# Kernel optimization log

Measured on AMD Instinct MI355X. Metric: run time of the kernel, lower is better.

The kernel has to match this reference:

```python
import jax, jax.numpy as jnp
import numpy as np

S = 64   # feature-map height/width = sqrt(qvk_dim)
M = 2    # memory_block_size


def _block_divide(t):
    # (b, c, S*S) -> (b, c, (S/M)**2, M*M), matching
    # Rearrange('b c (h m1) (w m2) -> b c (h w) (m1 m2)')
    b, c, _ = t.shape
    h = S // M
    t = t.reshape(b, c, h, M, h, M)
    t = jnp.transpose(t, (0, 1, 2, 4, 3, 5))
    return t.reshape(b, c, h * h, M * M)


def setup_inputs() -> dict:
    key = jax.random.key(0)
    k1, k2, k3, k4 = jax.random.split(key, 4)
    B, C, F = 64, 64, S * S
    x = jax.random.normal(k1, (B, C, F), dtype=jnp.float32)
    scale = 1.0 / np.sqrt(F)
    Wq = jax.random.normal(k2, (F, F), dtype=jnp.float32) * scale
    Wk = jax.random.normal(k3, (F, F), dtype=jnp.float32) * scale
    Wv = jax.random.normal(k4, (F, F), dtype=jnp.float32) * scale
    return {"x": x, "Wq": Wq, "Wk": Wk, "Wv": Wv}


def reference(x, Wq, Wk, Wv):
    # Linear(in, out, bias=False): y = x @ W.T, W: (out, in)
    q = _block_divide(jnp.einsum('bcf,qf->bcq', x, Wq))  # (b,c,n,g)
    k = _block_divide(jnp.einsum('bcf,qf->bcq', x, Wk))  # (b,c,n,p)
    v = _block_divide(jnp.einsum('bcf,qf->bcq', x, Wv))  # (b,c,n,p)
    # score[b,c,n,g,p] = q[b,c,n,g] * k[b,c,n,p]; softmax over p (dim=4)
    score = q[..., :, None] * k[..., None, :]             # (b,c,n,g,p)
    att = jax.nn.softmax(score, axis=-1)
    # matmul(att (g,p), v (p,1)) -> (g,1), then flatten blocks
    out = jnp.einsum('bcngp,bcnp->bcng', att, v)          # (b,c,n,g)
    b, c, n, g = out.shape
    return out.reshape(b, c, n * g)
```

## Files before the change

### kernel.cpp

```cpp
#include <hip/hip_runtime.h>

#define F        4096
#define NE       ((size_t)F * F)

typedef __attribute__((ext_vector_type(8))) short bf16x8;
typedef __attribute__((ext_vector_type(4))) float f32x4;

typedef const void __attribute__((address_space(1)))* gas1p;
typedef void __attribute__((address_space(3)))*       as3p;

__device__ __forceinline__ void gload16(const void* g, void* l) {
    __builtin_amdgcn_global_load_lds((gas1p)g, (as3p)l, 16, 0, 0);
}

__device__ __forceinline__ unsigned short f2bf(float f) {
    union { float f; unsigned int u; } c; c.f = f;
    unsigned int u = c.u;
    u += 0x7fffu + ((u >> 16) & 1u);
    return (unsigned short)(u >> 16);
}
__device__ __forceinline__ float bf2f(unsigned short u) {
    union { unsigned int u; float f; } c; c.u = ((unsigned int)u) << 16;
    return c.f;
}

__global__ void cvt_f32_bf16(const float* __restrict__ in,
                             unsigned short* __restrict__ out, int n4) {
    int idx    = blockIdx.x * blockDim.x + threadIdx.x;
    int stride = gridDim.x * blockDim.x;
    const float4* in4 = (const float4*)in;
    ushort4* out4 = (ushort4*)out;
    for (int i = idx; i < n4; i += stride) {
        float4 v = in4[i];
        ushort4 o;
        o.x = f2bf(v.x); o.y = f2bf(v.y); o.z = f2bf(v.z); o.w = f2bf(v.w);
        out4[i] = o;
    }
}

__device__ __forceinline__ int qo_map(int o) {
    int nblk = o >> 2, g = o & 3;
    return (nblk >> 5) * 128 + (g >> 1) * 64 + (nblk & 31) * 2 + (g & 1);
}

#define MFMA16(a, b, c) __builtin_amdgcn_mfma_f32_16x16x32_bf16(a, b, c, 0, 0, 0)

#define GBM 256
#define GBN 256
#define GBK 32
#define NKT (F / GBK)
#define ELPS (GBM * GBK)

__launch_bounds__(512, 1)
__global__ void gemm_qkv(const unsigned short* __restrict__ Xb,
                         const unsigned short* __restrict__ Qw,
                         const unsigned short* __restrict__ Kw,
                         const unsigned short* __restrict__ Vw,
                         unsigned short* __restrict__ qkv) {
    __shared__ __align__(16) unsigned short Als[4][GBM][GBK];
    __shared__ __align__(16) unsigned short Bls[4][GBN][GBK];

    const int tid  = threadIdx.x;
    const int lane = tid & 63;
    const int wid  = tid >> 6;
    const int wm   = wid >> 2;
    const int wn   = wid & 3;

    const int bid = blockIdx.x;
    const int swz = (bid & 7) * 96 + (bid >> 3);
    const int mt  = swz & 15;
    const int nt  = swz >> 4;
    const int bm  = mt * GBM;
    const int bnG = nt * GBN;
    const int mat = bnG >> 12;
    const int bn  = bnG & 4095;
    const unsigned short* __restrict__ Wsel = (mat == 0) ? Qw : (mat == 1) ? Kw : Vw;

    const int sr_row = tid >> 2;
    const int sr_chn = (tid & 3) ^ ((tid >> 3) & 3);
    const unsigned short* aSrc0 = Xb + (size_t)(bm + sr_row) * F + sr_chn * 8;
    const unsigned short* aSrc1 = aSrc0 + (size_t)128 * F;
    const unsigned short* bSrc0 = Wsel + (size_t)qo_map(bn + sr_row) * F + sr_chn * 8;
    const unsigned short* bSrc1 = Wsel + (size_t)qo_map(bn + 128 + sr_row) * F + sr_chn * 8;

#define STAGE_A(s, tt) do {                                                   \
        gload16(aSrc0 + (size_t)(tt) * GBK, (void*)&Als[s][wid * 16][0]);     \
        gload16(aSrc1 + (size_t)(tt) * GBK, (void*)&Als[s][128 + wid * 16][0]); \
    } while (0)
#define STAGE_B(s, tt) do {                                                   \
        gload16(bSrc0 + (size_t)(tt) * GBK, (void*)&Bls[s][wid * 16][0]);     \
        gload16(bSrc1 + (size_t)(tt) * GBK, (void*)&Bls[s][128 + wid * 16][0]); \
    } while (0)

    const int fr  = lane & 15;
    const int fq  = lane >> 4;
    const int fq2 = fq ^ ((fr >> 1) & 3);
    const unsigned short* aRd = &Als[0][wm * 128 + fr][fq2 * 8];
    const unsigned short* bRd = &Bls[0][wn * 64 + fr][fq2 * 8];

    f32x4 acc[8][4];
#pragma unroll
    for (int m = 0; m < 8; ++m)
#pragma unroll
        for (int n = 0; n < 4; ++n)
            acc[m][n] = (f32x4){0.f, 0.f, 0.f, 0.f};

    STAGE_A(0, 0); STAGE_B(0, 0);
    STAGE_A(1, 1); STAGE_B(1, 1);
    STAGE_A(2, 2); STAGE_B(2, 2);
    asm volatile("s_waitcnt vmcnt(8)" ::: "memory");
    __builtin_amdgcn_s_barrier();
    __builtin_amdgcn_sched_barrier(0);

#pragma unroll 4
    for (int t = 0; t < NKT; ++t) {
        const int s  = t & 3;
        const int ns = (t + 3) & 3;
        const int tt = (t + 3) & (NKT - 1);
        const unsigned short* aS = aRd + s * ELPS;
        const unsigned short* bS = bRd + s * ELPS;

        bf16x8 bf[4];
#pragma unroll
        for (int n = 0; n < 4; ++n) bf[n] = *(const bf16x8*)(bS + n * 512);
        bf16x8 af[4];
#pragma unroll
        for (int m = 0; m < 4; ++m) af[m] = *(const bf16x8*)(aS + m * 512);
        STAGE_A(ns, tt);
        __builtin_amdgcn_sched_barrier(0);
        __builtin_amdgcn_s_barrier();
        __builtin_amdgcn_s_setprio(1);
#pragma unroll
        for (int m = 0; m < 4; ++m)
#pragma unroll
            for (int n = 0; n < 4; ++n)
                acc[m][n] = MFMA16(af[m], bf[n], acc[m][n]);
        __builtin_amdgcn_s_setprio(0);
        __builtin_amdgcn_sched_barrier(0);
        __builtin_amdgcn_s_barrier();

#pragma unroll
        for (int m = 0; m < 4; ++m) af[m] = *(const bf16x8*)(aS + (4 + m) * 512);
        STAGE_B(ns, tt);
        __builtin_amdgcn_sched_barrier(0);
        __builtin_amdgcn_s_barrier();
        __builtin_amdgcn_s_setprio(1);
#pragma unroll
        for (int m = 0; m < 4; ++m)
#pragma unroll
            for (int n = 0; n < 4; ++n)
                acc[4 + m][n] = MFMA16(af[m], bf[n], acc[4 + m][n]);
        __builtin_amdgcn_s_setprio(0);
        asm volatile("s_waitcnt vmcnt(8)" ::: "memory");
        __builtin_amdgcn_sched_barrier(0);
        __builtin_amdgcn_s_barrier();
    }

    unsigned short* outB = qkv + (size_t)mat * NE;
#pragma unroll
    for (int m = 0; m < 8; ++m) {
#pragma unroll
        for (int n = 0; n < 4; ++n) {
#pragma unroll
            for (int r = 0; r < 4; ++r) {
                int row = bm + wm * 128 + m * 16 + fq * 4 + r;
                int col = bn + wn * 64 + n * 16 + fr;
                outB[(size_t)row * F + col] = f2bf(acc[m][n][r]);
            }
        }
    }
#undef STAGE_A
#undef STAGE_B
}

__global__ void attn_ep(const unsigned short* __restrict__ qkv,
                        float* __restrict__ out) {
    const size_t NB = NE / 4;
    const ushort4* q4 = (const ushort4*)qkv;
    const ushort4* k4 = q4 + NB;
    const ushort4* v4 = k4 + NB;
    float4* o4 = (float4*)out;
    size_t i      = (size_t)blockIdx.x * blockDim.x + threadIdx.x;
    size_t stride = (size_t)gridDim.x * blockDim.x;
    for (; i < NB; i += stride) {
        ushort4 qu = q4[i], ku = k4[i], vu = v4[i];
        float q0 = bf2f(qu.x), q1 = bf2f(qu.y), q2 = bf2f(qu.z), q3 = bf2f(qu.w);
        float k0 = bf2f(ku.x), k1 = bf2f(ku.y), k2 = bf2f(ku.z), k3 = bf2f(ku.w);
        float v0 = bf2f(vu.x), v1 = bf2f(vu.y), v2 = bf2f(vu.z), v3 = bf2f(vu.w);
        float4 res;
#pragma unroll
        for (int g = 0; g < 4; ++g) {
            float qg = (g == 0) ? q0 : (g == 1) ? q1 : (g == 2) ? q2 : q3;
            float s0 = qg * k0, s1 = qg * k1, s2 = qg * k2, s3 = qg * k3;
            float mx = fmaxf(fmaxf(s0, s1), fmaxf(s2, s3));
            float e0 = __expf(s0 - mx), e1 = __expf(s1 - mx);
            float e2 = __expf(s2 - mx), e3 = __expf(s3 - mx);
            float num = e0 * v0 + e1 * v1 + e2 * v2 + e3 * v3;
            float den = e0 + e1 + e2 + e3;
            float r = num / den;
            if (g == 0) res.x = r; else if (g == 1) res.y = r;
            else if (g == 2) res.z = r; else res.w = r;
        }
        o4[i] = res;
    }
}

#define BM       128
#define BN       128
#define BK       32
#define NTHREADS 512
#define KTILES   (F / BK)

__launch_bounds__(NTHREADS, 1)
__global__ void fused_qkv_attn(const unsigned short* __restrict__ Xb,
                               const unsigned short* __restrict__ Qw,
                               const unsigned short* __restrict__ Kw,
                               const unsigned short* __restrict__ Vw,
                               float* __restrict__ out) {
    __shared__ __align__(16) unsigned short Alds[BM][BK];
    __shared__ __align__(16) unsigned short Blds[3][BN][BK];

    const int tid  = threadIdx.x;
    const int lane = tid & 63;
    const int wid  = tid >> 6;
    const int wm   = wid >> 1;
    const int wn   = wid & 1;

    const int bm = blockIdx.y * BM;
    const int bn = blockIdx.x * BN;

    const int srow   = wid * 16 + (lane >> 2);
    const int kchunk = (lane & 3) ^ ((lane >> 3) & 3);
    const int scol   = kchunk * 8;

    const unsigned short* aG = Xb + (size_t)(bm + srow) * F + scol;
    const int o  = bn + srow;
    const int qo = qo_map(o);
    const unsigned short* qG = Qw + (size_t)qo * F + scol;
    const unsigned short* kG = Kw + (size_t)qo * F + scol;
    const unsigned short* vG = Vw + (size_t)qo * F + scol;

    unsigned short* aL = &Alds[wid * 16][0];
    unsigned short* qL = &Blds[0][wid * 16][0];
    unsigned short* kL = &Blds[1][wid * 16][0];
    unsigned short* vL = &Blds[2][wid * 16][0];

    const int fr  = lane & 15;
    const int fq  = lane >> 4;
    const int fq2 = fq ^ ((fr >> 1) & 3);

    const unsigned short* aP[2];
#pragma unroll
    for (int m = 0; m < 2; ++m)
        aP[m] = &Alds[wm * 32 + m * 16 + fr][fq2 * 8];
    const unsigned short* bP[4];
#pragma unroll
    for (int n = 0; n < 4; ++n)
        bP[n] = &Blds[0][wn * 64 + n * 16 + fr][fq2 * 8];

    f32x4 acc[3][2][4];
#pragma unroll
    for (int t = 0; t < 3; ++t)
#pragma unroll
        for (int m = 0; m < 2; ++m)
#pragma unroll
            for (int n = 0; n < 4; ++n)
                acc[t][m][n] = (f32x4){0.f, 0.f, 0.f, 0.f};

    for (int kt = 0; kt < KTILES; ++kt) {
        gload16(aG, aL);
        gload16(qG, qL);
        gload16(kG, kL);
        gload16(vG, vL);
        aG += BK; qG += BK; kG += BK; vG += BK;
        __syncthreads();

        bf16x8 afr[2];
#pragma unroll
        for (int m = 0; m < 2; ++m)
            afr[m] = *(const bf16x8*)aP[m];

#pragma unroll
        for (int t = 0; t < 3; ++t) {
#pragma unroll
            for (int n = 0; n < 4; ++n) {
                bf16x8 bfr = *(const bf16x8*)(bP[n] + t * (BN * BK));
#pragma unroll
                for (int m = 0; m < 2; ++m)
                    acc[t][m][n] = MFMA16(afr[m], bfr, acc[t][m][n]);
            }
        }
        __syncthreads();
    }

#pragma unroll
    for (int m = 0; m < 2; ++m) {
#pragma unroll
        for (int n = 0; n < 4; ++n) {
#pragma unroll
            for (int r = 0; r < 4; ++r) {
                float q  = acc[0][m][n][r];
                float k0 = acc[1][m][n][r];
                float v0 = acc[2][m][n][r];
                float k1 = __shfl_xor(k0, 1);
                float k2 = __shfl_xor(k0, 2);
                float k3 = __shfl_xor(k0, 3);
                float v1 = __shfl_xor(v0, 1);
                float v2 = __shfl_xor(v0, 2);
                float v3 = __shfl_xor(v0, 3);
                float s0 = q * k0, s1 = q * k1, s2 = q * k2, s3 = q * k3;
                float mx = fmaxf(fmaxf(s0, s1), fmaxf(s2, s3));
                float e0 = __expf(s0 - mx), e1 = __expf(s1 - mx);
                float e2 = __expf(s2 - mx), e3 = __expf(s3 - mx);
                float num = e0 * v0 + e1 * v1 + e2 * v2 + e3 * v3;
                float den = e0 + e1 + e2 + e3;
                int row = bm + wm * 32 + m * 16 + fq * 4 + r;
                int oc  = bn + wn * 64 + n * 16 + fr;
                out[(size_t)row * F + oc] = num / den;
            }
        }
    }
}

extern "C" void kernel_launch(void* const* d_in, const int* in_sizes, int n_in,
                              void* d_out, int out_size, void* d_ws, size_t ws_size,
                              hipStream_t stream) {
    const float* x  = (const float*)d_in[0];
    const float* Wq = (const float*)d_in[1];
    const float* Wk = (const float*)d_in[2];
    const float* Wv = (const float*)d_in[3];
    float* out = (float*)d_out;

    unsigned short* xb  = (unsigned short*)d_ws;
    unsigned short* wqb = xb  + NE;
    unsigned short* wkb = wqb + NE;
    unsigned short* wvb = wkb + NE;
    unsigned short* qkv = wvb + NE;

    const int n4 = (int)(NE / 4);
    cvt_f32_bf16<<<2048, 256, 0, stream>>>(x,  xb,  n4);
    cvt_f32_bf16<<<2048, 256, 0, stream>>>(Wq, wqb, n4);
    cvt_f32_bf16<<<2048, 256, 0, stream>>>(Wk, wkb, n4);
    cvt_f32_bf16<<<2048, 256, 0, stream>>>(Wv, wvb, n4);

    const size_t need_fast = NE * 2 * 7;
    if (ws_size >= need_fast) {
        gemm_qkv<<<768, 512, 0, stream>>>(xb, wqb, wkb, wvb, qkv);
        attn_ep<<<4096, 256, 0, stream>>>(qkv, out);
    } else {
        dim3 grid(F / BN, F / BM);
        fused_qkv_attn<<<grid, NTHREADS, 0, stream>>>(xb, wqb, wkb, wvb, out);
    }
}
```

Measured before the change: 487.6 us.

## Prefetch next LDS stage fragments during MFMA and merge conversion kernels

Restructures the GEMM main loop so the A and B fragments for the next k-step are read from LDS while the current step's MFMAs run. This drops the mid-iteration barriers and leaves a single barrier per iteration, with both global-to-LDS stages issued together and the wait count tightened. Separately, the four fp32-to-bf16 conversion launches become one launch with a 2D grid. In exchange it uses more registers (8 A fragments held across iterations), and the reworked barrier and waitcnt placement could expose LDS hazards or latency.

Result: faster. 465.9 us (-4.4%).

```diff
diff --git a/kernel.cpp b/kernel.cpp
--- a/kernel.cpp
+++ b/kernel.cpp
@@ -24,12 +24,19 @@
     return c.f;
 }
 
-__global__ void cvt_f32_bf16(const float* __restrict__ in,
-                             unsigned short* __restrict__ out, int n4) {
+__global__ void cvt_all(const float* __restrict__ s0, const float* __restrict__ s1,
+                        const float* __restrict__ s2, const float* __restrict__ s3,
+                        unsigned short* __restrict__ d0, unsigned short* __restrict__ d1,
+                        unsigned short* __restrict__ d2, unsigned short* __restrict__ d3,
+                        int n4) {
+    const float* src = (blockIdx.y == 0) ? s0 : (blockIdx.y == 1) ? s1
+                      : (blockIdx.y == 2) ? s2 : s3;
+    unsigned short* dst = (blockIdx.y == 0) ? d0 : (blockIdx.y == 1) ? d1
+                         : (blockIdx.y == 2) ? d2 : d3;
     int idx    = blockIdx.x * blockDim.x + threadIdx.x;
     int stride = gridDim.x * blockDim.x;
-    const float4* in4 = (const float4*)in;
-    ushort4* out4 = (ushort4*)out;
+    const float4* in4 = (const float4*)src;
+    ushort4* out4 = (ushort4*)dst;
     for (int i = idx; i < n4; i += stride) {
         float4 v = in4[i];
         ushort4 o;
@@ -83,12 +90,12 @@
     const unsigned short* bSrc0 = Wsel + (size_t)qo_map(bn + sr_row) * F + sr_chn * 8;
     const unsigned short* bSrc1 = Wsel + (size_t)qo_map(bn + 128 + sr_row) * F + sr_chn * 8;
 
-#define STAGE_A(s, tt) do {                                                   \
-        gload16(aSrc0 + (size_t)(tt) * GBK, (void*)&Als[s][wid * 16][0]);     \
+#define STAGE_A(s, tt) do {                                                     \
+        gload16(aSrc0 + (size_t)(tt) * GBK, (void*)&Als[s][wid * 16][0]);       \
         gload16(aSrc1 + (size_t)(tt) * GBK, (void*)&Als[s][128 + wid * 16][0]); \
     } while (0)
-#define STAGE_B(s, tt) do {                                                   \
-        gload16(bSrc0 + (size_t)(tt) * GBK, (void*)&Bls[s][wid * 16][0]);     \
+#define STAGE_B(s, tt) do {                                                     \
+        gload16(bSrc0 + (size_t)(tt) * GBK, (void*)&Bls[s][wid * 16][0]);       \
         gload16(bSrc1 + (size_t)(tt) * GBK, (void*)&Bls[s][128 + wid * 16][0]); \
     } while (0)
 
@@ -108,50 +115,41 @@
     STAGE_A(0, 0); STAGE_B(0, 0);
     STAGE_A(1, 1); STAGE_B(1, 1);
     STAGE_A(2, 2); STAGE_B(2, 2);
-    asm volatile("s_waitcnt vmcnt(8)" ::: "memory");
+    asm volatile("s_waitcnt vmcnt(4)" ::: "memory");
     __builtin_amdgcn_s_barrier();
     __builtin_amdgcn_sched_barrier(0);
 
+    bf16x8 af[8], bf[4];
+#pragma unroll
+    for (int m = 0; m < 8; ++m) af[m] = *(const bf16x8*)(aRd + m * 512);
+#pragma unroll
+    for (int n = 0; n < 4; ++n) bf[n] = *(const bf16x8*)(bRd + n * 512);
+
 #pragma unroll 4
     for (int t = 0; t < NKT; ++t) {
-        const int s  = t & 3;
-        const int ns = (t + 3) & 3;
+        const int sn = (t + 1) & 3;
+        const int ss = (t + 3) & 3;
         const int tt = (t + 3) & (NKT - 1);
-        const unsigned short* aS = aRd + s * ELPS;
-        const unsigned short* bS = bRd + s * ELPS;
-
-        bf16x8 bf[4];
-#pragma unroll
-        for (int n = 0; n < 4; ++n) bf[n] = *(const bf16x8*)(bS + n * 512);
-        bf16x8 af[4];
-#pragma unroll
-        for (int m = 0; m < 4; ++m) af[m] = *(const bf16x8*)(aS + m * 512);
-        STAGE_A(ns, tt);
-        __builtin_amdgcn_sched_barrier(0);
-        __builtin_amdgcn_s_barrier();
+        const unsigned short* aN = aRd + sn * ELPS;
+        const unsigned short* bN = bRd + sn * ELPS;
+
         __builtin_amdgcn_s_setprio(1);
 #pragma unroll
-        for (int m = 0; m < 4; ++m)
+        for (int m = 0; m < 8; ++m) {
 #pragma unroll
             for (int n = 0; n < 4; ++n)
                 acc[m][n] = MFMA16(af[m], bf[n], acc[m][n]);
+            af[m] = *(const bf16x8*)(aN + m * 512);
+        }
+#pragma unroll
+        for (int n = 0; n < 4; ++n)
+            bf[n] = *(const bf16x8*)(bN + n * 512);
         __builtin_amdgcn_s_setprio(0);
+
+        STAGE_A(ss, tt);
+        STAGE_B(ss, tt);
         __builtin_amdgcn_sched_barrier(0);
-        __builtin_amdgcn_s_barrier();
-
-#pragma unroll
-        for (int m = 0; m < 4; ++m) af[m] = *(const bf16x8*)(aS + (4 + m) * 512);
-        STAGE_B(ns, tt);
-        __builtin_amdgcn_sched_barrier(0);
-        __builtin_amdgcn_s_barrier();
-        __builtin_amdgcn_s_setprio(1);
-#pragma unroll
-        for (int m = 0; m < 4; ++m)
-#pragma unroll
-            for (int n = 0; n < 4; ++n)
-                acc[4 + m][n] = MFMA16(af[m], bf[n], acc[4 + m][n]);
-        __builtin_amdgcn_s_setprio(0);
-        asm volatile("s_waitcnt vmcnt(8)" ::: "memory");
+        asm volatile("s_waitcnt vmcnt(4)" ::: "memory");
         __builtin_amdgcn_sched_barrier(0);
         __builtin_amdgcn_s_barrier();
     }
@@ -338,10 +336,7 @@
     unsigned short* qkv = wvb + NE;
 
     const int n4 = (int)(NE / 4);
-    cvt_f32_bf16<<<2048, 256, 0, stream>>>(x,  xb,  n4);
-    cvt_f32_bf16<<<2048, 256, 0, stream>>>(Wq, wqb, n4);
-    cvt_f32_bf16<<<2048, 256, 0, stream>>>(Wk, wkb, n4);
-    cvt_f32_bf16<<<2048, 256, 0, stream>>>(Wv, wvb, n4);
+    cvt_all<<<dim3(2048, 4), 256, 0, stream>>>(x, Wq, Wk, Wv, xb, wqb, wkb, wvb, n4);
 
     const size_t need_fast = NE * 2 * 7;
     if (ws_size >= need_fast) {
```
